# Kernel tuning notes

Hardware: AMD Instinct MI355X
Metric: run time of the kernel (lower is better)

Reference implementation:

```python
import jax, jax.numpy as jnp
import numpy as np
import math

D_MODEL = 1024
N_HEADS = 16
D_HEAD = D_MODEL // N_HEADS  # 64, even (required for RoPE)
MAX_LEN = 1024


def _rope_cache(max_len, d_head, dtype=jnp.float32):
    half = d_head // 2
    inv_freq = jnp.exp(jnp.arange(half, dtype=dtype) * (-math.log(10000.0) / half))
    angles = jnp.arange(max_len, dtype=dtype)[:, None] * inv_freq[None, :]  # [max_len, half]
    return jnp.cos(angles), jnp.sin(angles)


def _apply_rope(t, cos, sin):
    # t: [B, H, L, D]; rotate-by-halves variant (cat of halves, not interleave)
    L = t.shape[2]
    half = t.shape[-1] // 2
    c = cos[:L, :half][None, None, :, :].astype(t.dtype)
    s = sin[:L, :half][None, None, :, :].astype(t.dtype)
    t1, t2 = t[..., :half], t[..., half:]
    return jnp.concatenate([t1 * c - t2 * s, t1 * s + t2 * c], axis=-1)


def setup_inputs() -> dict:
    key = jax.random.key(0)
    ks = jax.random.split(key, 11)
    B, L = 4, 1024
    std = 1.0 / math.sqrt(D_MODEL)
    return {
        "queries": jax.random.normal(ks[0], (B, L, D_MODEL), jnp.float32),
        "keys": jax.random.normal(ks[1], (B, L, D_MODEL), jnp.float32),
        "values": jax.random.normal(ks[2], (B, L, D_MODEL), jnp.float32),
        "Wq": jax.random.normal(ks[3], (D_MODEL, D_MODEL), jnp.float32) * std,
        "bq": jnp.zeros((D_MODEL,), jnp.float32),
        "Wk": jax.random.normal(ks[4], (D_MODEL, D_MODEL), jnp.float32) * std,
        "bk": jnp.zeros((D_MODEL,), jnp.float32),
        "Wv": jax.random.normal(ks[5], (D_MODEL, D_MODEL), jnp.float32) * std,
        "bv": jnp.zeros((D_MODEL,), jnp.float32),
        "Wo": jax.random.normal(ks[6], (D_MODEL, D_MODEL), jnp.float32) * std,
        "bo": jnp.zeros((D_MODEL,), jnp.float32),
    }


def reference(queries, keys, values, Wq, bq, Wk, bk, Wv, bv, Wo, bo):
    B, L, _ = queries.shape
    S = keys.shape[1]
    H, Dh = N_HEADS, D_HEAD
    cos, sin = _rope_cache(MAX_LEN, Dh, queries.dtype)

    q = (queries @ Wq + bq).reshape(B, L, H, Dh).transpose(0, 2, 1, 3)  # [B,H,L,Dh]
    k = (keys @ Wk + bk).reshape(B, S, H, Dh).transpose(0, 2, 1, 3)
    v = (values @ Wv + bv).reshape(B, S, H, Dh).transpose(0, 2, 1, 3)

    q = _apply_rope(q, cos, sin)
    k = _apply_rope(k, cos, sin)

    scores = jnp.einsum('bhid,bhjd->bhij', q, k) / math.sqrt(Dh)
    attn = jax.nn.softmax(scores, axis=-1)  # dropout is identity in eval
    out = jnp.einsum('bhij,bhjd->bhid', attn, v)  # [B,H,L,Dh]
    out = out.transpose(0, 2, 1, 3).reshape(B, L, H * Dh)
    return out @ Wo + bo
```

## Files before the change

kernel.cpp:

```cpp
#include <hip/hip_runtime.h>
#include <math.h>

#define BB 4
#define LL 1024
#define HH 16
#define DH 64
#define DM 1024
#define MM (BB * LL)

typedef short bf16x8 __attribute__((ext_vector_type(8)));
typedef float f32x4  __attribute__((ext_vector_type(4)));
typedef unsigned short u16x4 __attribute__((ext_vector_type(4)));

__device__ __forceinline__ unsigned short f2bf(float x) {
    union { float f; unsigned u; } v; v.f = x;
    unsigned r = v.u + 0x7fff + ((v.u >> 16) & 1);
    return (unsigned short)(r >> 16);
}

__device__ __forceinline__ void gl2lds16(const unsigned short* g, unsigned short* l) {
    __builtin_amdgcn_global_load_lds(
        (const __attribute__((address_space(1))) unsigned int*)g,
        (__attribute__((address_space(3))) unsigned int*)l, 16, 0, 0);
}

__device__ __forceinline__ void tile_map(int n, int& tM, int& tN) {
    tM = ((n >> 6) * 8 + (n & 7)) * 128;
    tN = ((n >> 3) & 7) * 128;
}

__global__ __launch_bounds__(256) void prep_kernel(
    const float* __restrict__ i0, const float* __restrict__ i1, const float* __restrict__ i2,
    unsigned short* __restrict__ o0, unsigned short* __restrict__ o1, unsigned short* __restrict__ o2,
    const float* __restrict__ w0, const float* __restrict__ w1,
    const float* __restrict__ w2, const float* __restrict__ w3,
    unsigned short* __restrict__ t0, unsigned short* __restrict__ t1,
    unsigned short* __restrict__ t2, unsigned short* __restrict__ t3,
    float* __restrict__ ct, float* __restrict__ st)
{
    const int z = blockIdx.z;
    const int bid = blockIdx.x, tid = threadIdx.x;

    if (z < 3) {
        const float* in = (z == 0) ? i0 : (z == 1) ? i1 : i2;
        unsigned short* out = (z == 0) ? o0 : (z == 1) ? o1 : o2;
        #pragma unroll
        for (int it = 0; it < 4; ++it) {
            size_t i = ((size_t)(it * 1024 + bid) * 256 + tid) * 4;
            float4 f = *(const float4*)(in + i);
            u16x4 r;
            r.x = f2bf(f.x); r.y = f2bf(f.y); r.z = f2bf(f.z); r.w = f2bf(f.w);
            *(u16x4*)(out + i) = r;
        }
    } else if (z == 3) {
        int idx = bid * 256 + tid;
        if (idx < LL * 32) {
            int l = idx >> 5, d = idx & 31;
            const float coef = -0.28782313662425583f;
            float ang = (float)l * expf((float)d * coef);
            float s, c;
            sincosf(ang, &s, &c);
            ct[idx] = c;
            st[idx] = s;
        }
    } else {
        const int w = z - 4;
        const float* in = (w == 0) ? w0 : (w == 1) ? w1 : (w == 2) ? w2 : w3;
        unsigned short* out = (w == 0) ? t0 : (w == 1) ? t1 : (w == 2) ? t2 : t3;
        __shared__ float tile[32][33];
        int tx = tid & 31, ty = tid >> 5;
        int c0 = (bid & 31) * 32, r0 = (bid >> 5) * 32;
        #pragma unroll
        for (int j = 0; j < 32; j += 8)
            tile[ty + j][tx] = in[(size_t)(r0 + ty + j) * 1024 + c0 + tx];
        __syncthreads();
        #pragma unroll
        for (int j = 0; j < 32; j += 8)
            out[(size_t)(c0 + ty + j) * 1024 + r0 + tx] = f2bf(tile[tx][ty + j]);
    }
}

__device__ __forceinline__ void gemm128_sb(
    const unsigned short* __restrict__ A, const unsigned short* __restrict__ Bt,
    unsigned short* As, unsigned short* Bs, int tM, int tN, f32x4 (&acc)[4][4])
{
    const int tid  = threadIdx.x;
    const int wave = tid >> 6, lane = tid & 63;
    const int g = lane >> 4, lm = lane & 15;
    const int wm = wave >> 1, wn = wave & 1;
    const int lr = lane >> 3, lk = lane & 7;
    const int kbl = lk ^ lr;

    for (int kt = 0; kt < 16; ++kt) {
        const int k0 = kt * 64;
        if (kt) __syncthreads();
        #pragma unroll
        for (int it = 0; it < 4; ++it) {
            int rbase = wave * 32 + it * 8;
            int r = rbase + lr;
            gl2lds16(A  + (size_t)(tM + r) * 1024 + k0 + kbl * 8, As + rbase * 64);
            gl2lds16(Bt + (size_t)(tN + r) * 1024 + k0 + kbl * 8, Bs + rbase * 64);
        }
        __syncthreads();

        #pragma unroll
        for (int kk = 0; kk < 2; ++kk) {
            bf16x8 a[4], b[4];
            const int sw = ((kk * 4 + g) ^ (lm & 7)) * 8;
            #pragma unroll
            for (int mt = 0; mt < 4; ++mt)
                a[mt] = *(const bf16x8*)&As[(wm * 64 + mt * 16 + lm) * 64 + sw];
            #pragma unroll
            for (int nt = 0; nt < 4; ++nt)
                b[nt] = *(const bf16x8*)&Bs[(wn * 64 + nt * 16 + lm) * 64 + sw];
            #pragma unroll
            for (int mt = 0; mt < 4; ++mt)
                #pragma unroll
                for (int nt = 0; nt < 4; ++nt)
                    acc[mt][nt] = __builtin_amdgcn_mfma_f32_16x16x32_bf16(
                        a[mt], b[nt], acc[mt][nt], 0, 0, 0);
        }
    }
}

__global__ __launch_bounds__(256) void gemm_qkv_kernel(
    const unsigned short* __restrict__ Aq, const unsigned short* __restrict__ Ak,
    const unsigned short* __restrict__ Av,
    const unsigned short* __restrict__ Wqt, const unsigned short* __restrict__ Wkt,
    const unsigned short* __restrict__ Wvt,
    const float* __restrict__ bq, const float* __restrict__ bk, const float* __restrict__ bv,
    const float* __restrict__ ct, const float* __restrict__ st,
    unsigned short* __restrict__ oq, unsigned short* __restrict__ ok,
    unsigned short* __restrict__ vt)
{
    __shared__ __align__(16) unsigned short As[128 * 64];
    __shared__ __align__(16) unsigned short Bs[128 * 64];

    const int z = blockIdx.z;
    const unsigned short* A  = (z == 0) ? Aq  : (z == 1) ? Ak  : Av;
    const unsigned short* Bt = (z == 0) ? Wqt : (z == 1) ? Wkt : Wvt;
    const float* bias        = (z == 0) ? bq  : (z == 1) ? bk  : bv;

    int tM, tN;
    tile_map(blockIdx.x, tM, tN);
    f32x4 acc[4][4] = {};
    gemm128_sb(A, Bt, As, Bs, tM, tN, acc);

    const int wave = threadIdx.x >> 6, lane = threadIdx.x & 63;
    const int g = lane >> 4, lm = lane & 15;
    const int wm = wave >> 1, wn = wave & 1;

    const int colbase = tN + wn * 64;
    const int h = colbase >> 6;
    float bvv[4];
    #pragma unroll
    for (int nt = 0; nt < 4; ++nt) bvv[nt] = bias[colbase + nt * 16 + lm];

    if (z == 2) {
        #pragma unroll
        for (int mt = 0; mt < 4; ++mt) {
            int row0 = tM + wm * 64 + mt * 16 + g * 4;
            int b = row0 >> 10, l0 = row0 & 1023;
            #pragma unroll
            for (int nt = 0; nt < 4; ++nt) {
                int dloc = nt * 16 + lm;
                u16x4 p4;
                #pragma unroll
                for (int r = 0; r < 4; ++r)
                    p4[r] = f2bf(acc[mt][nt][r] + bvv[nt]);
                *(u16x4*)(vt + (((size_t)(b * HH + h) * DH + dloc) << 10) + l0) = p4;
            }
        }
    } else {
        unsigned short* out = (z == 0) ? oq : ok;
        const float sc = (z == 0) ? 0.125f * 1.4426950408889634f : 1.0f;
        #pragma unroll
        for (int mt = 0; mt < 4; ++mt)
            #pragma unroll
            for (int r = 0; r < 4; ++r) {
                int row = tM + wm * 64 + mt * 16 + g * 4 + r;
                int b = row >> 10, l = row & 1023;
                const float* cl = ct + l * 32;
                const float* sl = st + l * 32;
                unsigned short* orow = out + ((size_t)(b * HH + h) * LL + l) * DH;
                #pragma unroll
                for (int nt = 0; nt < 2; ++nt) {
                    float t1 = acc[mt][nt][r]     + bvv[nt];
                    float t2 = acc[mt][nt + 2][r] + bvv[nt + 2];
                    float c = cl[nt * 16 + lm];
                    float s = sl[nt * 16 + lm];
                    orow[nt * 16 + lm]      = f2bf((t1 * c - t2 * s) * sc);
                    orow[nt * 16 + lm + 32] = f2bf((t1 * s + t2 * c) * sc);
                }
            }
    }
}

__global__ __launch_bounds__(256) void gemm_out_kernel(
    const unsigned short* __restrict__ A, const unsigned short* __restrict__ Bt,
    const float* __restrict__ bias, float* __restrict__ C)
{
    __shared__ __align__(16) unsigned short As[128 * 64];
    __shared__ __align__(16) unsigned short Bs[128 * 64];

    int tM, tN;
    tile_map(blockIdx.x, tM, tN);
    f32x4 acc[4][4] = {};
    gemm128_sb(A, Bt, As, Bs, tM, tN, acc);

    const int wave = threadIdx.x >> 6, lane = threadIdx.x & 63;
    const int g = lane >> 4, lm = lane & 15;
    const int wm = wave >> 1, wn = wave & 1;

    float bvv[4];
    #pragma unroll
    for (int nt = 0; nt < 4; ++nt) bvv[nt] = bias[tN + wn * 64 + nt * 16 + lm];
    #pragma unroll
    for (int mt = 0; mt < 4; ++mt)
        #pragma unroll
        for (int r = 0; r < 4; ++r) {
            int row = tM + wm * 64 + mt * 16 + g * 4 + r;
            float* crow = C + (size_t)row * DM + tN + wn * 64;
            #pragma unroll
            for (int nt = 0; nt < 4; ++nt)
                crow[nt * 16 + lm] = acc[mt][nt][r] + bvv[nt];
        }
}

#define PSTR 72

__global__ __launch_bounds__(256) void attn_mfma_kernel(
    const unsigned short* __restrict__ q, const unsigned short* __restrict__ k,
    const unsigned short* __restrict__ vt, unsigned short* __restrict__ ctx)
{
    __shared__ __align__(16) unsigned short Ks[64 * 64];
    __shared__ __align__(16) unsigned short Vs[64 * 64];
    __shared__ __align__(16) unsigned short Pb[4][16 * PSTR];

    const int tid  = threadIdx.x;
    const int wave = tid >> 6, lane = tid & 63;
    const int g = lane >> 4, lm = lane & 15;
    const int lr = lane >> 3, lk = lane & 7;
    const int kbl = lk ^ lr;
    const int n = blockIdx.x;
    const int bh = n & 63;
    const int qbase = (n >> 6) * 64;

    const unsigned short* qg  = q  + (size_t)(bh * LL + qbase) * DH;
    const unsigned short* kg  = k  + (size_t)bh * LL * DH;
    const unsigned short* vtg = vt + (size_t)bh * DH * LL;

    bf16x8 aq[2];
    {
        const unsigned short* qrow = qg + (wave * 16 + lm) * DH;
        aq[0] = *(const bf16x8*)(qrow + g * 8);
        aq[1] = *(const bf16x8*)(qrow + 32 + g * 8);
    }

    f32x4 acc[4] = {};
    float lsum = 0.f;

    for (int kt = 0; kt < 16; ++kt) {
        if (kt) __syncthreads();
        #pragma unroll
        for (int it = 0; it < 2; ++it) {
            int rbase = wave * 16 + it * 8;
            int r = rbase + lr;
            gl2lds16(kg  + (size_t)(kt * 64 + r) * DH + kbl * 8, Ks + rbase * 64);
            gl2lds16(vtg + (size_t)r * LL + kt * 64 + kbl * 8,  Vs + rbase * 64);
        }
        __syncthreads();

        f32x4 s[4] = {};
        #pragma unroll
        for (int kk = 0; kk < 2; ++kk) {
            const int sw = ((kk * 4 + g) ^ (lm & 7)) * 8;
            #pragma unroll
            for (int t = 0; t < 4; ++t) {
                bf16x8 ak = *(const bf16x8*)&Ks[(t * 16 + lm) * 64 + sw];
                s[t] = __builtin_amdgcn_mfma_f32_16x16x32_bf16(ak, aq[kk], s[t], 0, 0, 0);
            }
        }

        #pragma unroll
        for (int t = 0; t < 4; ++t) {
            u16x4 p4;
            #pragma unroll
            for (int r = 0; r < 4; ++r) {
                float p = exp2f(s[t][r]);
                lsum += p;
                p4[r] = f2bf(p);
            }
            *(u16x4*)&Pb[wave][lm * PSTR + t * 16 + g * 4] = p4;
        }

        #pragma unroll
        for (int kk = 0; kk < 2; ++kk) {
            const int sw = ((kk * 4 + g) ^ (lm & 7)) * 8;
            bf16x8 ap = *(const bf16x8*)&Pb[wave][lm * PSTR + kk * 32 + g * 8];
            #pragma unroll
            for (int dt = 0; dt < 4; ++dt) {
                bf16x8 bv = *(const bf16x8*)&Vs[(dt * 16 + lm) * 64 + sw];
                acc[dt] = __builtin_amdgcn_mfma_f32_16x16x32_bf16(ap, bv, acc[dt], 0, 0, 0);
            }
        }
    }

    float ts = lsum;
    ts += __shfl_xor(ts, 16, 64);
    ts += __shfl_xor(ts, 32, 64);

    int b = bh >> 4, h = bh & 15;
    #pragma unroll
    for (int r = 0; r < 4; ++r) {
        float inv = 1.f / __shfl(ts, g * 4 + r, 64);
        int qrow = qbase + wave * 16 + g * 4 + r;
        unsigned short* orow = ctx + (size_t)(b * LL + qrow) * DM + h * DH;
        #pragma unroll
        for (int dt = 0; dt < 4; ++dt)
            orow[dt * 16 + lm] = f2bf(acc[dt][r] * inv);
    }
}

extern "C" void kernel_launch(void* const* d_in, const int* in_sizes, int n_in,
                              void* d_out, int out_size, void* d_ws, size_t ws_size,
                              hipStream_t stream) {
    const float* queries = (const float*)d_in[0];
    const float* keys    = (const float*)d_in[1];
    const float* values  = (const float*)d_in[2];
    const float* Wq = (const float*)d_in[3];
    const float* bq = (const float*)d_in[4];
    const float* Wk = (const float*)d_in[5];
    const float* bk = (const float*)d_in[6];
    const float* Wv = (const float*)d_in[7];
    const float* bv = (const float*)d_in[8];
    const float* Wo = (const float*)d_in[9];
    const float* bo = (const float*)d_in[10];
    float* out = (float*)d_out;

    unsigned short* qb   = (unsigned short*)d_ws;
    unsigned short* kb_  = qb  + (size_t)MM * DM;
    unsigned short* vb_  = kb_ + (size_t)MM * DM;
    unsigned short* Wqt  = vb_ + (size_t)MM * DM;
    unsigned short* Wkt  = Wqt + (size_t)DM * DM;
    unsigned short* Wvt  = Wkt + (size_t)DM * DM;
    unsigned short* Wot  = Wvt + (size_t)DM * DM;
    unsigned short* q_ws = Wot + (size_t)DM * DM;
    unsigned short* k_ws = q_ws + (size_t)MM * DM;
    unsigned short* vt   = k_ws + (size_t)MM * DM;
    unsigned short* ctx  = vt   + (size_t)MM * DM;
    float* rope_cos = (float*)ctx;
    float* rope_sin = rope_cos + LL * 32;

    prep_kernel<<<dim3(1024, 1, 8), 256, 0, stream>>>(
        queries, keys, values, qb, kb_, vb_,
        Wq, Wk, Wv, Wo, Wqt, Wkt, Wvt, Wot, rope_cos, rope_sin);
    gemm_qkv_kernel<<<dim3(256, 1, 3), 256, 0, stream>>>(
        qb, kb_, vb_, Wqt, Wkt, Wvt, bq, bk, bv, rope_cos, rope_sin,
        q_ws, k_ws, vt);
    attn_mfma_kernel<<<dim3(LL / 64 * BB * HH), 256, 0, stream>>>(
        q_ws, k_ws, vt, ctx);
    gemm_out_kernel<<<dim3(256), 256, 0, stream>>>(
        ctx, Wot, bo, out);
}
```

Baseline: 215.4 us.

## Shrink GEMM tiles to 128x64 and pack softmax probabilities by truncation

Both GEMM kernels move from 128x128 to 128x64 output tiles. Each wave now owns two interleaved 16-column groups, so the RoPE pairing of columns d and d+32 stays inside a single thread. The grids grow from 256 to 512 blocks, which fills more of the many CUs on MI355X and lowers register and LDS pressure, at the cost of more reloads of the A operand. Separately, the attention kernel converts P to bf16 by byte-permute truncation instead of round-to-nearest, which is cheaper but slightly less precise.

```diff
diff --git a/kernel.cpp b/kernel.cpp
--- a/kernel.cpp
+++ b/kernel.cpp
@@ -11,6 +11,7 @@
 typedef short bf16x8 __attribute__((ext_vector_type(8)));
 typedef float f32x4  __attribute__((ext_vector_type(4)));
 typedef unsigned short u16x4 __attribute__((ext_vector_type(4)));
+typedef unsigned int   u32x2 __attribute__((ext_vector_type(2)));
 
 __device__ __forceinline__ unsigned short f2bf(float x) {
     union { float f; unsigned u; } v; v.f = x;
@@ -18,15 +19,19 @@
     return (unsigned short)(r >> 16);
 }
 
+__device__ __forceinline__ unsigned int fbits(float x) {
+    union { float f; unsigned u; } v; v.f = x; return v.u;
+}
+
 __device__ __forceinline__ void gl2lds16(const unsigned short* g, unsigned short* l) {
     __builtin_amdgcn_global_load_lds(
         (const __attribute__((address_space(1))) unsigned int*)g,
         (__attribute__((address_space(3))) unsigned int*)l, 16, 0, 0);
 }
 
-__device__ __forceinline__ void tile_map(int n, int& tM, int& tN) {
-    tM = ((n >> 6) * 8 + (n & 7)) * 128;
-    tN = ((n >> 3) & 7) * 128;
+__device__ __forceinline__ void tile_map64(int n, int& tM, int& tN) {
+    tM = ((n >> 7) * 8 + (n & 7)) * 128;
+    tN = ((n >> 3) & 15) * 64;
 }
 
 __global__ __launch_bounds__(256) void prep_kernel(
@@ -80,9 +85,9 @@
     }
 }
 
-__device__ __forceinline__ void gemm128_sb(
+__device__ __forceinline__ void gemm128x64_sb(
     const unsigned short* __restrict__ A, const unsigned short* __restrict__ Bt,
-    unsigned short* As, unsigned short* Bs, int tM, int tN, f32x4 (&acc)[4][4])
+    unsigned short* As, unsigned short* Bs, int tM, int tN, f32x4 (&acc)[4][2])
 {
     const int tid  = threadIdx.x;
     const int wave = tid >> 6, lane = tid & 63;
@@ -98,25 +103,30 @@
         for (int it = 0; it < 4; ++it) {
             int rbase = wave * 32 + it * 8;
             int r = rbase + lr;
-            gl2lds16(A  + (size_t)(tM + r) * 1024 + k0 + kbl * 8, As + rbase * 64);
+            gl2lds16(A + (size_t)(tM + r) * 1024 + k0 + kbl * 8, As + rbase * 64);
+        }
+        #pragma unroll
+        for (int it = 0; it < 2; ++it) {
+            int rbase = wave * 16 + it * 8;
+            int r = rbase + lr;
             gl2lds16(Bt + (size_t)(tN + r) * 1024 + k0 + kbl * 8, Bs + rbase * 64);
         }
         __syncthreads();
 
         #pragma unroll
         for (int kk = 0; kk < 2; ++kk) {
-            bf16x8 a[4], b[4];
+            bf16x8 a[4], b[2];
             const int sw = ((kk * 4 + g) ^ (lm & 7)) * 8;
             #pragma unroll
             for (int mt = 0; mt < 4; ++mt)
                 a[mt] = *(const bf16x8*)&As[(wm * 64 + mt * 16 + lm) * 64 + sw];
             #pragma unroll
-            for (int nt = 0; nt < 4; ++nt)
-                b[nt] = *(const bf16x8*)&Bs[(wn * 64 + nt * 16 + lm) * 64 + sw];
+            for (int nt = 0; nt < 2; ++nt)
+                b[nt] = *(const bf16x8*)&Bs[(wn * 16 + nt * 32 + lm) * 64 + sw];
             #pragma unroll
             for (int mt = 0; mt < 4; ++mt)
                 #pragma unroll
-                for (int nt = 0; nt < 4; ++nt)
+                for (int nt = 0; nt < 2; ++nt)
                     acc[mt][nt] = __builtin_amdgcn_mfma_f32_16x16x32_bf16(
                         a[mt], b[nt], acc[mt][nt], 0, 0, 0);
         }
@@ -134,7 +144,7 @@
     unsigned short* __restrict__ vt)
 {
     __shared__ __align__(16) unsigned short As[128 * 64];
-    __shared__ __align__(16) unsigned short Bs[128 * 64];
+    __shared__ __align__(16) unsigned short Bs[64 * 64];
 
     const int z = blockIdx.z;
     const unsigned short* A  = (z == 0) ? Aq  : (z == 1) ? Ak  : Av;
@@ -142,19 +152,18 @@
     const float* bias        = (z == 0) ? bq  : (z == 1) ? bk  : bv;
 
     int tM, tN;
-    tile_map(blockIdx.x, tM, tN);
-    f32x4 acc[4][4] = {};
-    gemm128_sb(A, Bt, As, Bs, tM, tN, acc);
+    tile_map64(blockIdx.x, tM, tN);
+    f32x4 acc[4][2] = {};
+    gemm128x64_sb(A, Bt, As, Bs, tM, tN, acc);
 
     const int wave = threadIdx.x >> 6, lane = threadIdx.x & 63;
     const int g = lane >> 4, lm = lane & 15;
     const int wm = wave >> 1, wn = wave & 1;
 
-    const int colbase = tN + wn * 64;
-    const int h = colbase >> 6;
-    float bvv[4];
+    const int h = tN >> 6;
+    float bvv[2];
     #pragma unroll
-    for (int nt = 0; nt < 4; ++nt) bvv[nt] = bias[colbase + nt * 16 + lm];
+    for (int nt = 0; nt < 2; ++nt) bvv[nt] = bias[tN + wn * 16 + nt * 32 + lm];
 
     if (z == 2) {
         #pragma unroll
@@ -162,8 +171,8 @@
             int row0 = tM + wm * 64 + mt * 16 + g * 4;
             int b = row0 >> 10, l0 = row0 & 1023;
             #pragma unroll
-            for (int nt = 0; nt < 4; ++nt) {
-                int dloc = nt * 16 + lm;
+            for (int nt = 0; nt < 2; ++nt) {
+                int dloc = wn * 16 + nt * 32 + lm;
                 u16x4 p4;
                 #pragma unroll
                 for (int r = 0; r < 4; ++r)
@@ -174,24 +183,20 @@
     } else {
         unsigned short* out = (z == 0) ? oq : ok;
         const float sc = (z == 0) ? 0.125f * 1.4426950408889634f : 1.0f;
+        const int dlo = wn * 16 + lm;
         #pragma unroll
         for (int mt = 0; mt < 4; ++mt)
             #pragma unroll
             for (int r = 0; r < 4; ++r) {
                 int row = tM + wm * 64 + mt * 16 + g * 4 + r;
                 int b = row >> 10, l = row & 1023;
-                const float* cl = ct + l * 32;
-                const float* sl = st + l * 32;
+                float c = ct[l * 32 + dlo];
+                float s = st[l * 32 + dlo];
                 unsigned short* orow = out + ((size_t)(b * HH + h) * LL + l) * DH;
-                #pragma unroll
-                for (int nt = 0; nt < 2; ++nt) {
-                    float t1 = acc[mt][nt][r]     + bvv[nt];
-                    float t2 = acc[mt][nt + 2][r] + bvv[nt + 2];
-                    float c = cl[nt * 16 + lm];
-                    float s = sl[nt * 16 + lm];
-                    orow[nt * 16 + lm]      = f2bf((t1 * c - t2 * s) * sc);
-                    orow[nt * 16 + lm + 32] = f2bf((t1 * s + t2 * c) * sc);
-                }
+                float t1 = acc[mt][0][r] + bvv[0];
+                float t2 = acc[mt][1][r] + bvv[1];
+                orow[dlo]      = f2bf((t1 * c - t2 * s) * sc);
+                orow[dlo + 32] = f2bf((t1 * s + t2 * c) * sc);
             }
     }
 }
@@ -201,29 +206,29 @@
     const float* __restrict__ bias, float* __restrict__ C)
 {
     __shared__ __align__(16) unsigned short As[128 * 64];
-    __shared__ __align__(16) unsigned short Bs[128 * 64];
+    __shared__ __align__(16) unsigned short Bs[64 * 64];
 
     int tM, tN;
-    tile_map(blockIdx.x, tM, tN);
-    f32x4 acc[4][4] = {};
-    gemm128_sb(A, Bt, As, Bs, tM, tN, acc);
+    tile_map64(blockIdx.x, tM, tN);
+    f32x4 acc[4][2] = {};
+    gemm128x64_sb(A, Bt, As, Bs, tM, tN, acc);
 
     const int wave = threadIdx.x >> 6, lane = threadIdx.x & 63;
     const int g = lane >> 4, lm = lane & 15;
     const int wm = wave >> 1, wn = wave & 1;
 
-    float bvv[4];
+    float bvv[2];
     #pragma unroll
-    for (int nt = 0; nt < 4; ++nt) bvv[nt] = bias[tN + wn * 64 + nt * 16 + lm];
+    for (int nt = 0; nt < 2; ++nt) bvv[nt] = bias[tN + wn * 16 + nt * 32 + lm];
     #pragma unroll
     for (int mt = 0; mt < 4; ++mt)
         #pragma unroll
         for (int r = 0; r < 4; ++r) {
             int row = tM + wm * 64 + mt * 16 + g * 4 + r;
-            float* crow = C + (size_t)row * DM + tN + wn * 64;
-            #pragma unroll
-            for (int nt = 0; nt < 4; ++nt)
-                crow[nt * 16 + lm] = acc[mt][nt][r] + bvv[nt];
+            float* crow = C + (size_t)row * DM + tN;
+            #pragma unroll
+            for (int nt = 0; nt < 2; ++nt)
+                crow[wn * 16 + nt * 32 + lm] = acc[mt][nt][r] + bvv[nt];
         }
 }
 
@@ -284,14 +289,13 @@
 
         #pragma unroll
         for (int t = 0; t < 4; ++t) {
-            u16x4 p4;
-            #pragma unroll
-            for (int r = 0; r < 4; ++r) {
-                float p = exp2f(s[t][r]);
-                lsum += p;
-                p4[r] = f2bf(p);
-            }
-            *(u16x4*)&Pb[wave][lm * PSTR + t * 16 + g * 4] = p4;
+            float p0 = exp2f(s[t][0]), p1 = exp2f(s[t][1]);
+            float p2 = exp2f(s[t][2]), p3 = exp2f(s[t][3]);
+            lsum += (p0 + p1) + (p2 + p3);
+            u32x2 pk;
+            pk[0] = __builtin_amdgcn_perm(fbits(p1), fbits(p0), 0x07060302u);
+            pk[1] = __builtin_amdgcn_perm(fbits(p3), fbits(p2), 0x07060302u);
+            *(u32x2*)&Pb[wave][lm * PSTR + t * 16 + g * 4] = pk;
         }
 
         #pragma unroll
@@ -355,11 +359,11 @@
     prep_kernel<<<dim3(1024, 1, 8), 256, 0, stream>>>(
         queries, keys, values, qb, kb_, vb_,
         Wq, Wk, Wv, Wo, Wqt, Wkt, Wvt, Wot, rope_cos, rope_sin);
-    gemm_qkv_kernel<<<dim3(256, 1, 3), 256, 0, stream>>>(
+    gemm_qkv_kernel<<<dim3(512, 1, 3), 256, 0, stream>>>(
         qb, kb_, vb_, Wqt, Wkt, Wvt, bq, bk, bv, rope_cos, rope_sin,
         q_ws, k_ws, vt);
     attn_mfma_kernel<<<dim3(LL / 64 * BB * HH), 256, 0, stream>>>(
         q_ws, k_ws, vt, ctx);
-    gemm_out_kernel<<<dim3(256), 256, 0, stream>>>(
+    gemm_out_kernel<<<dim3(512), 256, 0, stream>>>(
         ctx, Wot, bo, out);
 }
```

After: 207.9 us. 3.5% less time.
